# Optimization experiments

Hardware: AMD Instinct MI355X
Metric: run time of the kernel (lower is better)

Reference implementation:

```python
import jax, jax.numpy as jnp
import numpy as np

K = 64  # target active features per sample

def setup_inputs() -> dict:
    key = jax.random.key(0)
    x = jax.random.normal(key, (4096, 24576), dtype=jnp.float32)
    return {"x": x}

def reference(x) -> jnp.ndarray:
    # Training-mode BatchTopK: global threshold = min of top (k * batch) values
    # over the flattened batch, then ReLU(x) gated by (x >= threshold).
    batch_size = x.shape[0]
    total_k = min(K * batch_size, x.size)
    flat = x.reshape(-1)
    topv, _ = jax.lax.top_k(flat, total_k)
    threshold = jax.lax.stop_gradient(topv[-1])  # min of the top-k values (sorted desc)
    return jax.nn.relu(x) * (x >= threshold).astype(x.dtype)
```

## Files before the change

kernel.cpp:

```cpp
#include <hip/hip_runtime.h>

namespace {

struct SelState {
    unsigned forced_fb;
    unsigned bufcount;
    unsigned overflow;
    unsigned sel0;
    unsigned k1;
    unsigned sel1;
    unsigned k2;
};

constexpr int BINS12 = 4096;
constexpr int BINS8  = 256;
constexpr int LCAP   = 2048;
constexpr float GUESS = 2.5f;

using f4v = __attribute__((ext_vector_type(4))) float;

__device__ __forceinline__ unsigned f2key(float f) {
    unsigned u = __float_as_uint(f);
    return (u & 0x80000000u) ? ~u : (u | 0x80000000u);
}
__device__ __forceinline__ float key2f(unsigned k) {
    return __uint_as_float((k & 0x80000000u) ? (k & 0x7fffffffu) : ~k);
}
__device__ __forceinline__ bool is_fb(const SelState* st, unsigned total_k) {
    return st->forced_fb || st->overflow || (st->bufcount < total_k);
}

template <int NB>
__device__ __forceinline__ void scan_desc(const unsigned* __restrict__ hist, unsigned k,
                                          unsigned* __restrict__ lh, unsigned* __restrict__ res) {
    constexpr int CH = NB / 256;
    const int t = threadIdx.x;
    if (t == 0) { res[0] = 0; res[1] = k; }
    unsigned s = 0;
#pragma unroll
    for (int j = 0; j < CH; ++j) {
        unsigned c = hist[NB - 1 - (t * CH + j)];
        lh[t * CH + j] = c;
        s += c;
    }
    __syncthreads();
    const int lane = t & 63, wid = t >> 6;
    unsigned v = s;
#pragma unroll
    for (int d = 1; d < 64; d <<= 1) {
        unsigned u = __shfl_up(v, (unsigned)d, 64);
        if (lane >= d) v += u;
    }
    __shared__ unsigned wp[4];
    if (lane == 63) wp[wid] = v;
    __syncthreads();
    unsigned add = 0;
    for (int w = 0; w < wid; ++w) add += wp[w];
    v += add;
    unsigned pre = v - s;
    if (k > pre && k <= v) {
        unsigned cum = pre;
#pragma unroll
        for (int j = 0; j < CH; ++j) {
            unsigned c = lh[t * CH + j];
            if (cum + c >= k) { res[0] = (unsigned)(NB - 1 - (t * CH + j)); res[1] = k - cum; break; }
            cum += c;
        }
    }
    __syncthreads();
}

__global__ void init_kernel(unsigned* __restrict__ hist0, unsigned* __restrict__ hist1,
                            unsigned* __restrict__ hist2, SelState* __restrict__ st,
                            unsigned force_fb) {
    int t = blockIdx.x * blockDim.x + threadIdx.x;
    int stride = gridDim.x * blockDim.x;
    for (int i = t; i < BINS12; i += stride) { hist0[i] = 0; hist1[i] = 0; }
    if (t < BINS8) hist2[t] = 0;
    if (t == 0) {
        st->forced_fb = force_fb;
        st->bufcount = 0;
        st->overflow = 0;
    }
}

__global__ __launch_bounds__(256) void pass1_kernel(const float* __restrict__ x,
                                                    float* __restrict__ out, long long n,
                                                    unsigned* __restrict__ keys,
                                                    unsigned* __restrict__ idxs,
                                                    unsigned bufcap, SelState* __restrict__ st) {
    if (st->forced_fb) return;
    __shared__ unsigned lkey[LCAP];
    __shared__ unsigned lidx[LCAP];
    __shared__ unsigned lcnt;
    __shared__ unsigned gbase;
    if (threadIdx.x == 0) lcnt = 0;
    __syncthreads();

    const unsigned GKEY = f2key(GUESS);
    long long n4 = n >> 2;
    long long tid = (long long)blockIdx.x * blockDim.x + threadIdx.x;
    long long stride = (long long)gridDim.x * blockDim.x;
    const f4v* xv = (const f4v*)x;
    f4v* ov = (f4v*)out;
    f4v z4 = {0.f, 0.f, 0.f, 0.f};

    for (long long i = tid; i < n4; i += stride) {
        f4v v = __builtin_nontemporal_load(&xv[i]);
        __builtin_nontemporal_store(z4, &ov[i]);
#pragma unroll
        for (int c = 0; c < 4; ++c) {
            unsigned key = f2key(v[c]);
            if (key >= GKEY) {
                unsigned p = atomicAdd(&lcnt, 1u);
                if (p < LCAP) { lkey[p] = key; lidx[p] = (unsigned)((i << 2) + c); }
            }
        }
    }
    for (long long i = (n4 << 2) + tid; i < n; i += stride) {
        float v = x[i];
        out[i] = 0.f;
        unsigned key = f2key(v);
        if (key >= GKEY) {
            unsigned p = atomicAdd(&lcnt, 1u);
            if (p < LCAP) { lkey[p] = key; lidx[p] = (unsigned)i; }
        }
    }

    __syncthreads();
    unsigned cnt = lcnt;
    if (cnt > LCAP) cnt = LCAP;
    if (threadIdx.x == 0) {
        if (lcnt > LCAP) atomicOr(&st->overflow, 1u);
        unsigned base = atomicAdd(&st->bufcount, cnt);
        if (base + cnt > bufcap) atomicOr(&st->overflow, 1u);
        gbase = base;
    }
    __syncthreads();
    unsigned base = gbase;
    for (unsigned i = threadIdx.x; i < cnt; i += 256) {
        unsigned dst = base + i;
        if (dst < bufcap) { keys[dst] = lkey[i]; idxs[dst] = lidx[i]; }
    }
}

__global__ __launch_bounds__(256) void hist0_kernel(const float* __restrict__ x, long long n,
                                                    const unsigned* __restrict__ keys,
                                                    unsigned* __restrict__ hist0,
                                                    const SelState* __restrict__ st,
                                                    unsigned total_k) {
    __shared__ unsigned lh[BINS12];
    for (int i = threadIdx.x; i < BINS12; i += 256) lh[i] = 0;
    __syncthreads();

    long long tid = (long long)blockIdx.x * blockDim.x + threadIdx.x;
    long long stride = (long long)gridDim.x * blockDim.x;

    if (is_fb(st, total_k)) {
        long long n4 = n >> 2;
        const float4* x4 = (const float4*)x;
        for (long long i = tid; i < n4; i += stride) {
            float4 v = x4[i];
            float vv[4] = {v.x, v.y, v.z, v.w};
#pragma unroll
            for (int c = 0; c < 4; ++c) atomicAdd(&lh[f2key(vv[c]) >> 20], 1u);
        }
        for (long long i = (n4 << 2) + tid; i < n; i += stride)
            atomicAdd(&lh[f2key(x[i]) >> 20], 1u);
    } else {
        long long cnt = (long long)st->bufcount;
        long long c4 = cnt >> 2;
        const uint4* k4 = (const uint4*)keys;
        for (long long i = tid; i < c4; i += stride) {
            uint4 kv = k4[i];
            atomicAdd(&lh[kv.x >> 20], 1u);
            atomicAdd(&lh[kv.y >> 20], 1u);
            atomicAdd(&lh[kv.z >> 20], 1u);
            atomicAdd(&lh[kv.w >> 20], 1u);
        }
        for (long long i = (c4 << 2) + tid; i < cnt; i += stride)
            atomicAdd(&lh[keys[i] >> 20], 1u);
    }

    __syncthreads();
    for (int i = threadIdx.x; i < BINS12; i += 256) {
        unsigned c = lh[i];
        if (c) atomicAdd(&hist0[i], c);
    }
}

__global__ __launch_bounds__(256) void hist1_kernel(const float* __restrict__ x, long long n,
                                                    const unsigned* __restrict__ keys,
                                                    const unsigned* __restrict__ hist0,
                                                    unsigned* __restrict__ hist1,
                                                    SelState* __restrict__ st,
                                                    unsigned total_k) {
    __shared__ unsigned lh[BINS12];
    __shared__ unsigned res[2];
    scan_desc<BINS12>(hist0, total_k, lh, res);
    const unsigned sel0 = res[0];
    if (threadIdx.x == 0 && blockIdx.x == 0) { st->sel0 = sel0; st->k1 = res[1]; }

    for (int i = threadIdx.x; i < BINS12; i += 256) lh[i] = 0;
    __syncthreads();

    long long tid = (long long)blockIdx.x * blockDim.x + threadIdx.x;
    long long stride = (long long)gridDim.x * blockDim.x;

    if (is_fb(st, total_k)) {
        long long n4 = n >> 2;
        const float4* x4 = (const float4*)x;
        for (long long i = tid; i < n4; i += stride) {
            float4 v = x4[i];
            float vv[4] = {v.x, v.y, v.z, v.w};
#pragma unroll
            for (int c = 0; c < 4; ++c) {
                unsigned key = f2key(vv[c]);
                if ((key >> 20) == sel0) atomicAdd(&lh[(key >> 8) & 0xFFFu], 1u);
            }
        }
        for (long long i = (n4 << 2) + tid; i < n; i += stride) {
            unsigned key = f2key(x[i]);
            if ((key >> 20) == sel0) atomicAdd(&lh[(key >> 8) & 0xFFFu], 1u);
        }
    } else {
        long long cnt = (long long)st->bufcount;
        long long c4 = cnt >> 2;
        const uint4* k4 = (const uint4*)keys;
        for (long long i = tid; i < c4; i += stride) {
            uint4 kv = k4[i];
            unsigned kk[4] = {kv.x, kv.y, kv.z, kv.w};
#pragma unroll
            for (int c = 0; c < 4; ++c)
                if ((kk[c] >> 20) == sel0) atomicAdd(&lh[(kk[c] >> 8) & 0xFFFu], 1u);
        }
        for (long long i = (c4 << 2) + tid; i < cnt; i += stride) {
            unsigned key = keys[i];
            if ((key >> 20) == sel0) atomicAdd(&lh[(key >> 8) & 0xFFFu], 1u);
        }
    }

    __syncthreads();
    for (int i = threadIdx.x; i < BINS12; i += 256) {
        unsigned c = lh[i];
        if (c) atomicAdd(&hist1[i], c);
    }
}

__global__ __launch_bounds__(256) void hist2_kernel(const float* __restrict__ x, long long n,
                                                    const unsigned* __restrict__ keys,
                                                    const unsigned* __restrict__ hist1,
                                                    unsigned* __restrict__ hist2,
                                                    SelState* __restrict__ st,
                                                    unsigned total_k) {
    __shared__ unsigned lh[BINS12];
    __shared__ unsigned res[2];
    scan_desc<BINS12>(hist1, st->k1, lh, res);
    const unsigned sel1 = (st->sel0 << 12) | res[0];
    if (threadIdx.x == 0 && blockIdx.x == 0) { st->sel1 = sel1; st->k2 = res[1]; }

    for (int i = threadIdx.x; i < BINS8; i += 256) lh[i] = 0;
    __syncthreads();

    long long tid = (long long)blockIdx.x * blockDim.x + threadIdx.x;
    long long stride = (long long)gridDim.x * blockDim.x;

    if (is_fb(st, total_k)) {
        long long n4 = n >> 2;
        const float4* x4 = (const float4*)x;
        for (long long i = tid; i < n4; i += stride) {
            float4 v = x4[i];
            float vv[4] = {v.x, v.y, v.z, v.w};
#pragma unroll
            for (int c = 0; c < 4; ++c) {
                unsigned key = f2key(vv[c]);
                if ((key >> 8) == sel1) atomicAdd(&lh[key & 0xFFu], 1u);
            }
        }
        for (long long i = (n4 << 2) + tid; i < n; i += stride) {
            unsigned key = f2key(x[i]);
            if ((key >> 8) == sel1) atomicAdd(&lh[key & 0xFFu], 1u);
        }
    } else {
        long long cnt = (long long)st->bufcount;
        long long c4 = cnt >> 2;
        const uint4* k4 = (const uint4*)keys;
        for (long long i = tid; i < c4; i += stride) {
            uint4 kv = k4[i];
            unsigned kk[4] = {kv.x, kv.y, kv.z, kv.w};
#pragma unroll
            for (int c = 0; c < 4; ++c)
                if ((kk[c] >> 8) == sel1) atomicAdd(&lh[kk[c] & 0xFFu], 1u);
        }
        for (long long i = (c4 << 2) + tid; i < cnt; i += stride) {
            unsigned key = keys[i];
            if ((key >> 8) == sel1) atomicAdd(&lh[key & 0xFFu], 1u);
        }
    }

    __syncthreads();
    for (int i = threadIdx.x; i < BINS8; i += 256) {
        unsigned c = lh[i];
        if (c) atomicAdd(&hist2[i], c);
    }
}

__global__ __launch_bounds__(256) void gate_kernel(const float* __restrict__ x,
                                                   float* __restrict__ out, long long n,
                                                   const unsigned* __restrict__ keys,
                                                   const unsigned* __restrict__ idxs,
                                                   const unsigned* __restrict__ hist2,
                                                   const SelState* __restrict__ st,
                                                   unsigned total_k) {
    __shared__ unsigned lh[BINS8];
    __shared__ unsigned res[2];
    scan_desc<BINS8>(hist2, st->k2, lh, res);
    const unsigned tkey = (st->sel1 << 8) | res[0];

    long long tid = (long long)blockIdx.x * blockDim.x + threadIdx.x;
    long long stride = (long long)gridDim.x * blockDim.x;

    if (is_fb(st, total_k)) {
        float thr = key2f(tkey);
        long long n4 = n >> 2;
        const float4* x4 = (const float4*)x;
        float4* o4 = (float4*)out;
        for (long long i = tid; i < n4; i += stride) {
            float4 v = x4[i];
            float4 r;
            r.x = (v.x >= thr) ? fmaxf(v.x, 0.f) : 0.f;
            r.y = (v.y >= thr) ? fmaxf(v.y, 0.f) : 0.f;
            r.z = (v.z >= thr) ? fmaxf(v.z, 0.f) : 0.f;
            r.w = (v.w >= thr) ? fmaxf(v.w, 0.f) : 0.f;
            o4[i] = r;
        }
        for (long long i = (n4 << 2) + tid; i < n; i += stride) {
            float v = x[i];
            out[i] = (v >= thr) ? fmaxf(v, 0.f) : 0.f;
        }
    } else {
        long long cnt = (long long)st->bufcount;
        for (long long i = tid; i < cnt; i += stride) {
            unsigned kk = keys[i];
            if (kk >= tkey) out[idxs[i]] = key2f(kk);
        }
    }
}

}

extern "C" void kernel_launch(void* const* d_in, const int* in_sizes, int n_in,
                              void* d_out, int out_size, void* d_ws, size_t ws_size,
                              hipStream_t stream) {
    const float* x = (const float*)d_in[0];
    float* out = (float*)d_out;
    long long n = (long long)in_sizes[0];

    long long tk = 64LL * 4096LL;
    if (tk > n) tk = n;
    unsigned total_k = (unsigned)tk;

    char* ws = (char*)d_ws;
    unsigned* hist0 = (unsigned*)(ws);
    unsigned* hist1 = (unsigned*)(ws + 16384);
    unsigned* hist2 = (unsigned*)(ws + 32768);
    SelState* st    = (SelState*)(ws + 33792);

    unsigned bufcap = 0;
    unsigned* keys = (unsigned*)(ws + 65536);
    unsigned* idxs = nullptr;
    if (ws_size > 65536) {
        size_t avail = (ws_size - 65536) / 8;
        size_t cap = avail > 16u * 1024u * 1024u ? 16u * 1024u * 1024u : avail;
        bufcap = (unsigned)(cap & ~3ull);
        idxs = keys + bufcap;
    }
    unsigned force_fb = (bufcap < 2u * total_k || n > 0xFFFF0000LL) ? 1u : 0u;

    const int blocks = 2048;

    init_kernel<<<16, 256, 0, stream>>>(hist0, hist1, hist2, st, force_fb);
    pass1_kernel<<<blocks, 256, 0, stream>>>(x, out, n, keys, idxs, bufcap, st);
    hist0_kernel<<<blocks, 256, 0, stream>>>(x, n, keys, hist0, st, total_k);
    hist1_kernel<<<blocks, 256, 0, stream>>>(x, n, keys, hist0, hist1, st, total_k);
    hist2_kernel<<<blocks, 256, 0, stream>>>(x, n, keys, hist1, hist2, st, total_k);
    gate_kernel<<<blocks, 256, 0, stream>>>(x, out, n, keys, idxs, hist2, st, total_k);
}
```

Baseline: 209.7 us.

## Fuse top-bin histogram into candidate pass and zero output via memset

The first-level 12-bit histogram is now built inside the candidate-collection pass using a shared-memory histogram, so the separate pass over the candidate buffer is no longer needed on the fast path. The fallback path keeps its own histogram kernel, which writes to a separate buffer, and hist1 chooses which of the two to scan. Output zeroing moves out of pass1 into a hipMemsetAsync, so pass1 now only reads the input. The trade-off is an extra 16 KB of LDS per block in pass1, which may lower occupancy, and an extra fill operation on the stream.

```diff
diff --git a/kernel.cpp b/kernel.cpp
--- a/kernel.cpp
+++ b/kernel.cpp
@@ -70,12 +70,12 @@
     __syncthreads();
 }
 
-__global__ void init_kernel(unsigned* __restrict__ hist0, unsigned* __restrict__ hist1,
-                            unsigned* __restrict__ hist2, SelState* __restrict__ st,
-                            unsigned force_fb) {
+__global__ void init_kernel(unsigned* __restrict__ hist0s, unsigned* __restrict__ hist0f,
+                            unsigned* __restrict__ hist1, unsigned* __restrict__ hist2,
+                            SelState* __restrict__ st, unsigned force_fb) {
     int t = blockIdx.x * blockDim.x + threadIdx.x;
     int stride = gridDim.x * blockDim.x;
-    for (int i = t; i < BINS12; i += stride) { hist0[i] = 0; hist1[i] = 0; }
+    for (int i = t; i < BINS12; i += stride) { hist0s[i] = 0; hist0f[i] = 0; hist1[i] = 0; }
     if (t < BINS8) hist2[t] = 0;
     if (t == 0) {
         st->forced_fb = force_fb;
@@ -84,16 +84,19 @@
     }
 }
 
-__global__ __launch_bounds__(256) void pass1_kernel(const float* __restrict__ x,
-                                                    float* __restrict__ out, long long n,
+__global__ __launch_bounds__(256) void pass1_kernel(const float* __restrict__ x, long long n,
                                                     unsigned* __restrict__ keys,
                                                     unsigned* __restrict__ idxs,
-                                                    unsigned bufcap, SelState* __restrict__ st) {
+                                                    unsigned bufcap,
+                                                    unsigned* __restrict__ hist0s,
+                                                    SelState* __restrict__ st) {
     if (st->forced_fb) return;
     __shared__ unsigned lkey[LCAP];
     __shared__ unsigned lidx[LCAP];
+    __shared__ unsigned lhist[BINS12];
     __shared__ unsigned lcnt;
     __shared__ unsigned gbase;
+    for (int i = threadIdx.x; i < BINS12; i += 256) lhist[i] = 0;
     if (threadIdx.x == 0) lcnt = 0;
     __syncthreads();
 
@@ -102,28 +105,25 @@
     long long tid = (long long)blockIdx.x * blockDim.x + threadIdx.x;
     long long stride = (long long)gridDim.x * blockDim.x;
     const f4v* xv = (const f4v*)x;
-    f4v* ov = (f4v*)out;
-    f4v z4 = {0.f, 0.f, 0.f, 0.f};
 
     for (long long i = tid; i < n4; i += stride) {
         f4v v = __builtin_nontemporal_load(&xv[i]);
-        __builtin_nontemporal_store(z4, &ov[i]);
 #pragma unroll
         for (int c = 0; c < 4; ++c) {
             unsigned key = f2key(v[c]);
             if (key >= GKEY) {
                 unsigned p = atomicAdd(&lcnt, 1u);
                 if (p < LCAP) { lkey[p] = key; lidx[p] = (unsigned)((i << 2) + c); }
+                atomicAdd(&lhist[key >> 20], 1u);
             }
         }
     }
     for (long long i = (n4 << 2) + tid; i < n; i += stride) {
-        float v = x[i];
-        out[i] = 0.f;
-        unsigned key = f2key(v);
+        unsigned key = f2key(x[i]);
         if (key >= GKEY) {
             unsigned p = atomicAdd(&lcnt, 1u);
             if (p < LCAP) { lkey[p] = key; lidx[p] = (unsigned)i; }
+            atomicAdd(&lhist[key >> 20], 1u);
         }
     }
 
@@ -142,62 +142,50 @@
         unsigned dst = base + i;
         if (dst < bufcap) { keys[dst] = lkey[i]; idxs[dst] = lidx[i]; }
     }
-}
-
-__global__ __launch_bounds__(256) void hist0_kernel(const float* __restrict__ x, long long n,
-                                                    const unsigned* __restrict__ keys,
-                                                    unsigned* __restrict__ hist0,
-                                                    const SelState* __restrict__ st,
-                                                    unsigned total_k) {
+    for (int i = threadIdx.x; i < BINS12; i += 256) {
+        unsigned c = lhist[i];
+        if (c) atomicAdd(&hist0s[i], c);
+    }
+}
+
+__global__ __launch_bounds__(256) void fb_hist0_kernel(const float* __restrict__ x, long long n,
+                                                       unsigned* __restrict__ hist0f,
+                                                       const SelState* __restrict__ st,
+                                                       unsigned total_k) {
+    if (!is_fb(st, total_k)) return;
     __shared__ unsigned lh[BINS12];
     for (int i = threadIdx.x; i < BINS12; i += 256) lh[i] = 0;
     __syncthreads();
-
-    long long tid = (long long)blockIdx.x * blockDim.x + threadIdx.x;
-    long long stride = (long long)gridDim.x * blockDim.x;
-
-    if (is_fb(st, total_k)) {
-        long long n4 = n >> 2;
-        const float4* x4 = (const float4*)x;
-        for (long long i = tid; i < n4; i += stride) {
-            float4 v = x4[i];
-            float vv[4] = {v.x, v.y, v.z, v.w};
-#pragma unroll
-            for (int c = 0; c < 4; ++c) atomicAdd(&lh[f2key(vv[c]) >> 20], 1u);
-        }
-        for (long long i = (n4 << 2) + tid; i < n; i += stride)
-            atomicAdd(&lh[f2key(x[i]) >> 20], 1u);
-    } else {
-        long long cnt = (long long)st->bufcount;
-        long long c4 = cnt >> 2;
-        const uint4* k4 = (const uint4*)keys;
-        for (long long i = tid; i < c4; i += stride) {
-            uint4 kv = k4[i];
-            atomicAdd(&lh[kv.x >> 20], 1u);
-            atomicAdd(&lh[kv.y >> 20], 1u);
-            atomicAdd(&lh[kv.z >> 20], 1u);
-            atomicAdd(&lh[kv.w >> 20], 1u);
-        }
-        for (long long i = (c4 << 2) + tid; i < cnt; i += stride)
-            atomicAdd(&lh[keys[i] >> 20], 1u);
-    }
-
+    long long n4 = n >> 2;
+    long long tid = (long long)blockIdx.x * blockDim.x + threadIdx.x;
+    long long stride = (long long)gridDim.x * blockDim.x;
+    const float4* x4 = (const float4*)x;
+    for (long long i = tid; i < n4; i += stride) {
+        float4 v = x4[i];
+        float vv[4] = {v.x, v.y, v.z, v.w};
+#pragma unroll
+        for (int c = 0; c < 4; ++c) atomicAdd(&lh[f2key(vv[c]) >> 20], 1u);
+    }
+    for (long long i = (n4 << 2) + tid; i < n; i += stride)
+        atomicAdd(&lh[f2key(x[i]) >> 20], 1u);
     __syncthreads();
     for (int i = threadIdx.x; i < BINS12; i += 256) {
         unsigned c = lh[i];
-        if (c) atomicAdd(&hist0[i], c);
+        if (c) atomicAdd(&hist0f[i], c);
     }
 }
 
 __global__ __launch_bounds__(256) void hist1_kernel(const float* __restrict__ x, long long n,
                                                     const unsigned* __restrict__ keys,
-                                                    const unsigned* __restrict__ hist0,
+                                                    const unsigned* __restrict__ hist0s,
+                                                    const unsigned* __restrict__ hist0f,
                                                     unsigned* __restrict__ hist1,
                                                     SelState* __restrict__ st,
                                                     unsigned total_k) {
     __shared__ unsigned lh[BINS12];
     __shared__ unsigned res[2];
-    scan_desc<BINS12>(hist0, total_k, lh, res);
+    const bool fb = is_fb(st, total_k);
+    scan_desc<BINS12>(fb ? hist0f : hist0s, total_k, lh, res);
     const unsigned sel0 = res[0];
     if (threadIdx.x == 0 && blockIdx.x == 0) { st->sel0 = sel0; st->k1 = res[1]; }
 
@@ -207,7 +195,7 @@
     long long tid = (long long)blockIdx.x * blockDim.x + threadIdx.x;
     long long stride = (long long)gridDim.x * blockDim.x;
 
-    if (is_fb(st, total_k)) {
+    if (fb) {
         long long n4 = n >> 2;
         const float4* x4 = (const float4*)x;
         for (long long i = tid; i < n4; i += stride) {
@@ -361,10 +349,11 @@
     unsigned total_k = (unsigned)tk;
 
     char* ws = (char*)d_ws;
-    unsigned* hist0 = (unsigned*)(ws);
-    unsigned* hist1 = (unsigned*)(ws + 16384);
-    unsigned* hist2 = (unsigned*)(ws + 32768);
-    SelState* st    = (SelState*)(ws + 33792);
+    unsigned* hist0s = (unsigned*)(ws);
+    unsigned* hist0f = (unsigned*)(ws + 16384);
+    unsigned* hist1  = (unsigned*)(ws + 32768);
+    unsigned* hist2  = (unsigned*)(ws + 49152);
+    SelState* st     = (SelState*)(ws + 50176);
 
     unsigned bufcap = 0;
     unsigned* keys = (unsigned*)(ws + 65536);
@@ -379,10 +368,11 @@
 
     const int blocks = 2048;
 
-    init_kernel<<<16, 256, 0, stream>>>(hist0, hist1, hist2, st, force_fb);
-    pass1_kernel<<<blocks, 256, 0, stream>>>(x, out, n, keys, idxs, bufcap, st);
-    hist0_kernel<<<blocks, 256, 0, stream>>>(x, n, keys, hist0, st, total_k);
-    hist1_kernel<<<blocks, 256, 0, stream>>>(x, n, keys, hist0, hist1, st, total_k);
+    hipMemsetAsync(out, 0, (size_t)n * sizeof(float), stream);
+    init_kernel<<<16, 256, 0, stream>>>(hist0s, hist0f, hist1, hist2, st, force_fb);
+    pass1_kernel<<<blocks, 256, 0, stream>>>(x, n, keys, idxs, bufcap, hist0s, st);
+    fb_hist0_kernel<<<blocks, 256, 0, stream>>>(x, n, hist0f, st, total_k);
+    hist1_kernel<<<blocks, 256, 0, stream>>>(x, n, keys, hist0s, hist0f, hist1, st, total_k);
     hist2_kernel<<<blocks, 256, 0, stream>>>(x, n, keys, hist1, hist2, st, total_k);
     gate_kernel<<<blocks, 256, 0, stream>>>(x, out, n, keys, idxs, hist2, st, total_k);
 }
```

After: 211.5 us. No clear change (+0.9%).

## Fuse radix-select pipeline into one cooperative kernel with grid syncs

Applied to the files above, without the earlier changes.

Replaces the six-kernel chain (init, candidate gather, three histogram passes, gate) with a single cooperative persistent kernel that uses grid.sync between phases. Each block redoes the histogram prefix scans locally instead of passing selections through global state. The output zeroing is split from the candidate scan into its own store loop. Launch overhead and inter-kernel gaps go away, at the cost of grid-wide barriers and a grid limited to the resident block count. The old chain is kept as a fallback if the cooperative launch fails.

```diff
diff --git a/kernel.cpp b/kernel.cpp
--- a/kernel.cpp
+++ b/kernel.cpp
@@ -1,4 +1,7 @@
 #include <hip/hip_runtime.h>
+#include <hip/hip_cooperative_groups.h>
+
+namespace cg = cooperative_groups;
 
 namespace {
 
@@ -70,6 +73,208 @@
     __syncthreads();
 }
 
+template <int SHIFT, int MASK>
+__device__ __forceinline__ void hist_accum_x(const float* __restrict__ x, long long n,
+                                             unsigned sel, int selshift,
+                                             unsigned* __restrict__ lh,
+                                             long long tid, long long stride) {
+    long long n4 = n >> 2;
+    const float4* x4 = (const float4*)x;
+    for (long long i = tid; i < n4; i += stride) {
+        float4 v = x4[i];
+        float vv[4] = {v.x, v.y, v.z, v.w};
+#pragma unroll
+        for (int c = 0; c < 4; ++c) {
+            unsigned key = f2key(vv[c]);
+            if (selshift == 32 || (key >> selshift) == sel)
+                atomicAdd(&lh[(key >> SHIFT) & MASK], 1u);
+        }
+    }
+    for (long long i = (n4 << 2) + tid; i < n; i += stride) {
+        unsigned key = f2key(x[i]);
+        if (selshift == 32 || (key >> selshift) == sel)
+            atomicAdd(&lh[(key >> SHIFT) & MASK], 1u);
+    }
+}
+template <int SHIFT, int MASK>
+__device__ __forceinline__ void hist_accum_keys(const unsigned* __restrict__ keys, long long cnt,
+                                                unsigned sel, int selshift,
+                                                unsigned* __restrict__ lh,
+                                                long long tid, long long stride) {
+    long long c4 = cnt >> 2;
+    const uint4* k4 = (const uint4*)keys;
+    for (long long i = tid; i < c4; i += stride) {
+        uint4 kv = k4[i];
+        unsigned kk[4] = {kv.x, kv.y, kv.z, kv.w};
+#pragma unroll
+        for (int c = 0; c < 4; ++c)
+            if (selshift == 32 || (kk[c] >> selshift) == sel)
+                atomicAdd(&lh[(kk[c] >> SHIFT) & MASK], 1u);
+    }
+    for (long long i = (c4 << 2) + tid; i < cnt; i += stride) {
+        unsigned key = keys[i];
+        if (selshift == 32 || (key >> selshift) == sel)
+            atomicAdd(&lh[(key >> SHIFT) & MASK], 1u);
+    }
+}
+
+__global__ __launch_bounds__(256, 4) void mega_kernel(
+    const float* __restrict__ x, float* __restrict__ out, long long n,
+    unsigned* __restrict__ keys, unsigned* __restrict__ idxs, unsigned bufcap,
+    unsigned* __restrict__ hist0, unsigned* __restrict__ hist1,
+    unsigned* __restrict__ hist2, SelState* __restrict__ st,
+    unsigned total_k, unsigned force_fb) {
+    cg::grid_group grid = cg::this_grid();
+    __shared__ unsigned smem[BINS12];
+    unsigned* lkey = smem;
+    unsigned* lidx = smem + LCAP;
+    unsigned* lh   = smem;
+    __shared__ unsigned lcnt, gbase, sfb, scnt;
+    __shared__ unsigned res[2];
+
+    const int t = threadIdx.x;
+    const long long tid = (long long)blockIdx.x * blockDim.x + t;
+    const long long stride = (long long)gridDim.x * blockDim.x;
+
+    for (long long i = tid; i < BINS12; i += stride) { hist0[i] = 0; hist1[i] = 0; }
+    for (long long i = tid; i < BINS8; i += stride) hist2[i] = 0;
+    if (tid == 0) { st->bufcount = 0; st->overflow = 0; }
+    grid.sync();
+
+    {
+        f4v z = {0.f, 0.f, 0.f, 0.f};
+        long long n4 = n >> 2;
+        f4v* ov = (f4v*)out;
+        for (long long i = tid; i < n4; i += stride) __builtin_nontemporal_store(z, &ov[i]);
+        for (long long i = (n4 << 2) + tid; i < n; i += stride) out[i] = 0.f;
+    }
+    if (!force_fb) {
+        if (t == 0) lcnt = 0;
+        __syncthreads();
+        const unsigned GKEY = f2key(GUESS);
+        long long n8 = n >> 3;
+        const f4v* xv = (const f4v*)x;
+        for (long long i = tid; i < n8; i += stride) {
+            f4v a = __builtin_nontemporal_load(&xv[2 * i]);
+            f4v b = __builtin_nontemporal_load(&xv[2 * i + 1]);
+#pragma unroll
+            for (int c = 0; c < 4; ++c) {
+                unsigned key = f2key(a[c]);
+                if (key >= GKEY) {
+                    unsigned p = atomicAdd(&lcnt, 1u);
+                    if (p < LCAP) { lkey[p] = key; lidx[p] = (unsigned)((i << 3) + c); }
+                }
+            }
+#pragma unroll
+            for (int c = 0; c < 4; ++c) {
+                unsigned key = f2key(b[c]);
+                if (key >= GKEY) {
+                    unsigned p = atomicAdd(&lcnt, 1u);
+                    if (p < LCAP) { lkey[p] = key; lidx[p] = (unsigned)((i << 3) + 4 + c); }
+                }
+            }
+        }
+        for (long long i = (n8 << 3) + tid; i < n; i += stride) {
+            unsigned key = f2key(x[i]);
+            if (key >= GKEY) {
+                unsigned p = atomicAdd(&lcnt, 1u);
+                if (p < LCAP) { lkey[p] = key; lidx[p] = (unsigned)i; }
+            }
+        }
+        __syncthreads();
+        unsigned cnt = lcnt > LCAP ? LCAP : lcnt;
+        if (t == 0) {
+            if (lcnt > LCAP) atomicOr(&st->overflow, 1u);
+            unsigned base = atomicAdd(&st->bufcount, cnt);
+            if (base + cnt > bufcap) atomicOr(&st->overflow, 1u);
+            gbase = base;
+        }
+        __syncthreads();
+        unsigned base = gbase;
+        for (unsigned i = t; i < cnt; i += 256) {
+            unsigned dst = base + i;
+            if (dst < bufcap) { keys[dst] = lkey[i]; idxs[dst] = lidx[i]; }
+        }
+    }
+    grid.sync();
+
+    if (t == 0) {
+        unsigned ov = atomicOr(&st->overflow, 0u);
+        unsigned bc = atomicAdd(&st->bufcount, 0u);
+        sfb = (force_fb || ov || bc < total_k) ? 1u : 0u;
+        scnt = bc < bufcap ? bc : bufcap;
+    }
+    __syncthreads();
+    const bool fb = (sfb != 0u);
+    const long long cnt = (long long)scnt;
+
+    for (int i = t; i < BINS12; i += 256) lh[i] = 0;
+    __syncthreads();
+    if (fb) hist_accum_x<20, 0xFFF>(x, n, 0, 32, lh, tid, stride);
+    else    hist_accum_keys<20, 0xFFF>(keys, cnt, 0, 32, lh, tid, stride);
+    __syncthreads();
+    for (int i = t; i < BINS12; i += 256) {
+        unsigned c = lh[i];
+        if (c) atomicAdd(&hist0[i], c);
+    }
+    grid.sync();
+
+    scan_desc<BINS12>(hist0, total_k, lh, res);
+    const unsigned sel0 = res[0];
+    const unsigned k1 = res[1];
+    for (int i = t; i < BINS12; i += 256) lh[i] = 0;
+    __syncthreads();
+    if (fb) hist_accum_x<8, 0xFFF>(x, n, sel0, 20, lh, tid, stride);
+    else    hist_accum_keys<8, 0xFFF>(keys, cnt, sel0, 20, lh, tid, stride);
+    __syncthreads();
+    for (int i = t; i < BINS12; i += 256) {
+        unsigned c = lh[i];
+        if (c) atomicAdd(&hist1[i], c);
+    }
+    grid.sync();
+
+    scan_desc<BINS12>(hist1, k1, lh, res);
+    const unsigned sel1 = (sel0 << 12) | res[0];
+    const unsigned k2 = res[1];
+    for (int i = t; i < BINS8; i += 256) lh[i] = 0;
+    __syncthreads();
+    if (fb) hist_accum_x<0, 0xFF>(x, n, sel1, 8, lh, tid, stride);
+    else    hist_accum_keys<0, 0xFF>(keys, cnt, sel1, 8, lh, tid, stride);
+    __syncthreads();
+    for (int i = t; i < BINS8; i += 256) {
+        unsigned c = lh[i];
+        if (c) atomicAdd(&hist2[i], c);
+    }
+    grid.sync();
+
+    scan_desc<BINS8>(hist2, k2, lh, res);
+    const unsigned tkey = (sel1 << 8) | res[0];
+    if (fb) {
+        float thr = key2f(tkey);
+        long long n4 = n >> 2;
+        const float4* x4 = (const float4*)x;
+        float4* o4 = (float4*)out;
+        for (long long i = tid; i < n4; i += stride) {
+            float4 v = x4[i];
+            float4 r;
+            r.x = (v.x >= thr) ? fmaxf(v.x, 0.f) : 0.f;
+            r.y = (v.y >= thr) ? fmaxf(v.y, 0.f) : 0.f;
+            r.z = (v.z >= thr) ? fmaxf(v.z, 0.f) : 0.f;
+            r.w = (v.w >= thr) ? fmaxf(v.w, 0.f) : 0.f;
+            o4[i] = r;
+        }
+        for (long long i = (n4 << 2) + tid; i < n; i += stride) {
+            float v = x[i];
+            out[i] = (v >= thr) ? fmaxf(v, 0.f) : 0.f;
+        }
+    } else {
+        for (long long i = tid; i < cnt; i += stride) {
+            unsigned kk = keys[i];
+            if (kk >= tkey) out[idxs[i]] = key2f(kk);
+        }
+    }
+}
+
 __global__ void init_kernel(unsigned* __restrict__ hist0, unsigned* __restrict__ hist1,
                             unsigned* __restrict__ hist2, SelState* __restrict__ st,
                             unsigned force_fb) {
@@ -77,26 +282,19 @@
     int stride = gridDim.x * blockDim.x;
     for (int i = t; i < BINS12; i += stride) { hist0[i] = 0; hist1[i] = 0; }
     if (t < BINS8) hist2[t] = 0;
-    if (t == 0) {
-        st->forced_fb = force_fb;
-        st->bufcount = 0;
-        st->overflow = 0;
-    }
-}
-
-__global__ __launch_bounds__(256) void pass1_kernel(const float* __restrict__ x,
-                                                    float* __restrict__ out, long long n,
-                                                    unsigned* __restrict__ keys,
-                                                    unsigned* __restrict__ idxs,
-                                                    unsigned bufcap, SelState* __restrict__ st) {
-    if (st->forced_fb) return;
+    if (t == 0) { st->forced_fb = force_fb; st->bufcount = 0; st->overflow = 0; }
+}
+
+__global__ __launch_bounds__(256) void pass1_chain(const float* __restrict__ x,
+                                                   float* __restrict__ out, long long n,
+                                                   unsigned* __restrict__ keys,
+                                                   unsigned* __restrict__ idxs,
+                                                   unsigned bufcap, SelState* __restrict__ st) {
     __shared__ unsigned lkey[LCAP];
     __shared__ unsigned lidx[LCAP];
-    __shared__ unsigned lcnt;
-    __shared__ unsigned gbase;
+    __shared__ unsigned lcnt, gbase;
     if (threadIdx.x == 0) lcnt = 0;
     __syncthreads();
-
     const unsigned GKEY = f2key(GUESS);
     long long n4 = n >> 2;
     long long tid = (long long)blockIdx.x * blockDim.x + threadIdx.x;
@@ -104,7 +302,6 @@
     const f4v* xv = (const f4v*)x;
     f4v* ov = (f4v*)out;
     f4v z4 = {0.f, 0.f, 0.f, 0.f};
-
     for (long long i = tid; i < n4; i += stride) {
         f4v v = __builtin_nontemporal_load(&xv[i]);
         __builtin_nontemporal_store(z4, &ov[i]);
@@ -126,10 +323,8 @@
             if (p < LCAP) { lkey[p] = key; lidx[p] = (unsigned)i; }
         }
     }
-
-    __syncthreads();
-    unsigned cnt = lcnt;
-    if (cnt > LCAP) cnt = LCAP;
+    __syncthreads();
+    unsigned cnt = lcnt > LCAP ? LCAP : lcnt;
     if (threadIdx.x == 0) {
         if (lcnt > LCAP) atomicOr(&st->overflow, 1u);
         unsigned base = atomicAdd(&st->bufcount, cnt);
@@ -144,44 +339,18 @@
     }
 }
 
-__global__ __launch_bounds__(256) void hist0_kernel(const float* __restrict__ x, long long n,
-                                                    const unsigned* __restrict__ keys,
-                                                    unsigned* __restrict__ hist0,
-                                                    const SelState* __restrict__ st,
-                                                    unsigned total_k) {
+__global__ __launch_bounds__(256) void hist0_chain(const float* __restrict__ x, long long n,
+                                                   const unsigned* __restrict__ keys,
+                                                   unsigned* __restrict__ hist0,
+                                                   const SelState* __restrict__ st,
+                                                   unsigned total_k) {
     __shared__ unsigned lh[BINS12];
     for (int i = threadIdx.x; i < BINS12; i += 256) lh[i] = 0;
     __syncthreads();
-
     long long tid = (long long)blockIdx.x * blockDim.x + threadIdx.x;
     long long stride = (long long)gridDim.x * blockDim.x;
-
-    if (is_fb(st, total_k)) {
-        long long n4 = n >> 2;
-        const float4* x4 = (const float4*)x;
-        for (long long i = tid; i < n4; i += stride) {
-            float4 v = x4[i];
-            float vv[4] = {v.x, v.y, v.z, v.w};
-#pragma unroll
-            for (int c = 0; c < 4; ++c) atomicAdd(&lh[f2key(vv[c]) >> 20], 1u);
-        }
-        for (long long i = (n4 << 2) + tid; i < n; i += stride)
-            atomicAdd(&lh[f2key(x[i]) >> 20], 1u);
-    } else {
-        long long cnt = (long long)st->bufcount;
-        long long c4 = cnt >> 2;
-        const uint4* k4 = (const uint4*)keys;
-        for (long long i = tid; i < c4; i += stride) {
-            uint4 kv = k4[i];
-            atomicAdd(&lh[kv.x >> 20], 1u);
-            atomicAdd(&lh[kv.y >> 20], 1u);
-            atomicAdd(&lh[kv.z >> 20], 1u);
-            atomicAdd(&lh[kv.w >> 20], 1u);
-        }
-        for (long long i = (c4 << 2) + tid; i < cnt; i += stride)
-            atomicAdd(&lh[keys[i] >> 20], 1u);
-    }
-
+    if (is_fb(st, total_k)) hist_accum_x<20, 0xFFF>(x, n, 0, 32, lh, tid, stride);
+    else hist_accum_keys<20, 0xFFF>(keys, (long long)(st->bufcount < 0x7FFFFFFFu ? st->bufcount : 0), 0, 32, lh, tid, stride);
     __syncthreads();
     for (int i = threadIdx.x; i < BINS12; i += 256) {
         unsigned c = lh[i];
@@ -189,57 +358,23 @@
     }
 }
 
-__global__ __launch_bounds__(256) void hist1_kernel(const float* __restrict__ x, long long n,
-                                                    const unsigned* __restrict__ keys,
-                                                    const unsigned* __restrict__ hist0,
-                                                    unsigned* __restrict__ hist1,
-                                                    SelState* __restrict__ st,
-                                                    unsigned total_k) {
+__global__ __launch_bounds__(256) void hist1_chain(const float* __restrict__ x, long long n,
+                                                   const unsigned* __restrict__ keys,
+                                                   const unsigned* __restrict__ hist0,
+                                                   unsigned* __restrict__ hist1,
+                                                   SelState* __restrict__ st,
+                                                   unsigned total_k) {
     __shared__ unsigned lh[BINS12];
     __shared__ unsigned res[2];
     scan_desc<BINS12>(hist0, total_k, lh, res);
     const unsigned sel0 = res[0];
     if (threadIdx.x == 0 && blockIdx.x == 0) { st->sel0 = sel0; st->k1 = res[1]; }
-
     for (int i = threadIdx.x; i < BINS12; i += 256) lh[i] = 0;
     __syncthreads();
-
     long long tid = (long long)blockIdx.x * blockDim.x + threadIdx.x;
     long long stride = (long long)gridDim.x * blockDim.x;
-
-    if (is_fb(st, total_k)) {
-        long long n4 = n >> 2;
-        const float4* x4 = (const float4*)x;
-        for (long long i = tid; i < n4; i += stride) {
-            float4 v = x4[i];
-            float vv[4] = {v.x, v.y, v.z, v.w};
-#pragma unroll
-            for (int c = 0; c < 4; ++c) {
-                unsigned key = f2key(vv[c]);
-                if ((key >> 20) == sel0) atomicAdd(&lh[(key >> 8) & 0xFFFu], 1u);
-            }
-        }
-        for (long long i = (n4 << 2) + tid; i < n; i += stride) {
-            unsigned key = f2key(x[i]);
-            if ((key >> 20) == sel0) atomicAdd(&lh[(key >> 8) & 0xFFFu], 1u);
-        }
-    } else {
-        long long cnt = (long long)st->bufcount;
-        long long c4 = cnt >> 2;
-        const uint4* k4 = (const uint4*)keys;
-        for (long long i = tid; i < c4; i += stride) {
-            uint4 kv = k4[i];
-            unsigned kk[4] = {kv.x, kv.y, kv.z, kv.w};
-#pragma unroll
-            for (int c = 0; c < 4; ++c)
-                if ((kk[c] >> 20) == sel0) atomicAdd(&lh[(kk[c] >> 8) & 0xFFFu], 1u);
-        }
-        for (long long i = (c4 << 2) + tid; i < cnt; i += stride) {
-            unsigned key = keys[i];
-            if ((key >> 20) == sel0) atomicAdd(&lh[(key >> 8) & 0xFFFu], 1u);
-        }
-    }
-
+    if (is_fb(st, total_k)) hist_accum_x<8, 0xFFF>(x, n, sel0, 20, lh, tid, stride);
+    else hist_accum_keys<8, 0xFFF>(keys, (long long)st->bufcount, sel0, 20, lh, tid, stride);
     __syncthreads();
     for (int i = threadIdx.x; i < BINS12; i += 256) {
         unsigned c = lh[i];
@@ -247,57 +382,23 @@
     }
 }
 
-__global__ __launch_bounds__(256) void hist2_kernel(const float* __restrict__ x, long long n,
-                                                    const unsigned* __restrict__ keys,
-                                                    const unsigned* __restrict__ hist1,
-                                                    unsigned* __restrict__ hist2,
-                                                    SelState* __restrict__ st,
-                                                    unsigned total_k) {
+__global__ __launch_bounds__(256) void hist2_chain(const float* __restrict__ x, long long n,
+                                                   const unsigned* __restrict__ keys,
+                                                   const unsigned* __restrict__ hist1,
+                                                   unsigned* __restrict__ hist2,
+                                                   SelState* __restrict__ st,
+                                                   unsigned total_k) {
     __shared__ unsigned lh[BINS12];
     __shared__ unsigned res[2];
     scan_desc<BINS12>(hist1, st->k1, lh, res);
     const unsigned sel1 = (st->sel0 << 12) | res[0];
     if (threadIdx.x == 0 && blockIdx.x == 0) { st->sel1 = sel1; st->k2 = res[1]; }
-
     for (int i = threadIdx.x; i < BINS8; i += 256) lh[i] = 0;
     __syncthreads();
-
     long long tid = (long long)blockIdx.x * blockDim.x + threadIdx.x;
     long long stride = (long long)gridDim.x * blockDim.x;
-
-    if (is_fb(st, total_k)) {
-        long long n4 = n >> 2;
-        const float4* x4 = (const float4*)x;
-        for (long long i = tid; i < n4; i += stride) {
-            float4 v = x4[i];
-            float vv[4] = {v.x, v.y, v.z, v.w};
-#pragma unroll
-            for (int c = 0; c < 4; ++c) {
-                unsigned key = f2key(vv[c]);
-                if ((key >> 8) == sel1) atomicAdd(&lh[key & 0xFFu], 1u);
-            }
-        }
-        for (long long i = (n4 << 2) + tid; i < n; i += stride) {
-            unsigned key = f2key(x[i]);
-            if ((key >> 8) == sel1) atomicAdd(&lh[key & 0xFFu], 1u);
-        }
-    } else {
-        long long cnt = (long long)st->bufcount;
-        long long c4 = cnt >> 2;
-        const uint4* k4 = (const uint4*)keys;
-        for (long long i = tid; i < c4; i += stride) {
-            uint4 kv = k4[i];
-            unsigned kk[4] = {kv.x, kv.y, kv.z, kv.w};
-#pragma unroll
-            for (int c = 0; c < 4; ++c)
-                if ((kk[c] >> 8) == sel1) atomicAdd(&lh[kk[c] & 0xFFu], 1u);
-        }
-        for (long long i = (c4 << 2) + tid; i < cnt; i += stride) {
-            unsigned key = keys[i];
-            if ((key >> 8) == sel1) atomicAdd(&lh[key & 0xFFu], 1u);
-        }
-    }
-
+    if (is_fb(st, total_k)) hist_accum_x<0, 0xFF>(x, n, sel1, 8, lh, tid, stride);
+    else hist_accum_keys<0, 0xFF>(keys, (long long)st->bufcount, sel1, 8, lh, tid, stride);
     __syncthreads();
     for (int i = threadIdx.x; i < BINS8; i += 256) {
         unsigned c = lh[i];
@@ -305,21 +406,19 @@
     }
 }
 
-__global__ __launch_bounds__(256) void gate_kernel(const float* __restrict__ x,
-                                                   float* __restrict__ out, long long n,
-                                                   const unsigned* __restrict__ keys,
-                                                   const unsigned* __restrict__ idxs,
-                                                   const unsigned* __restrict__ hist2,
-                                                   const SelState* __restrict__ st,
-                                                   unsigned total_k) {
+__global__ __launch_bounds__(256) void gate_chain(const float* __restrict__ x,
+                                                  float* __restrict__ out, long long n,
+                                                  const unsigned* __restrict__ keys,
+                                                  const unsigned* __restrict__ idxs,
+                                                  const unsigned* __restrict__ hist2,
+                                                  const SelState* __restrict__ st,
+                                                  unsigned total_k) {
     __shared__ unsigned lh[BINS8];
     __shared__ unsigned res[2];
     scan_desc<BINS8>(hist2, st->k2, lh, res);
     const unsigned tkey = (st->sel1 << 8) | res[0];
-
     long long tid = (long long)blockIdx.x * blockDim.x + threadIdx.x;
     long long stride = (long long)gridDim.x * blockDim.x;
-
     if (is_fb(st, total_k)) {
         float thr = key2f(tkey);
         long long n4 = n >> 2;
@@ -377,12 +476,29 @@
     }
     unsigned force_fb = (bufcap < 2u * total_k || n > 0xFFFF0000LL) ? 1u : 0u;
 
+    int dev = 0;
+    hipGetDevice(&dev);
+    int cus = 0;
+    hipDeviceGetAttribute(&cus, hipDeviceAttributeMultiprocessorCount, dev);
+    int maxb = 0;
+    hipOccupancyMaxActiveBlocksPerMultiprocessor(&maxb, (const void*)mega_kernel, 256, 0);
+    long long capacity = (long long)maxb * (long long)cus;
+
+    if (capacity >= 256) {
+        int grid = (int)(capacity > 4096 ? 4096 : capacity);
+        void* args[] = {(void*)&x, (void*)&out, (void*)&n, (void*)&keys, (void*)&idxs,
+                        (void*)&bufcap, (void*)&hist0, (void*)&hist1, (void*)&hist2,
+                        (void*)&st, (void*)&total_k, (void*)&force_fb};
+        hipError_t e = hipLaunchCooperativeKernel((const void*)mega_kernel, dim3(grid),
+                                                  dim3(256), args, 0, stream);
+        if (e == hipSuccess) return;
+    }
+
     const int blocks = 2048;
-
     init_kernel<<<16, 256, 0, stream>>>(hist0, hist1, hist2, st, force_fb);
-    pass1_kernel<<<blocks, 256, 0, stream>>>(x, out, n, keys, idxs, bufcap, st);
-    hist0_kernel<<<blocks, 256, 0, stream>>>(x, n, keys, hist0, st, total_k);
-    hist1_kernel<<<blocks, 256, 0, stream>>>(x, n, keys, hist0, hist1, st, total_k);
-    hist2_kernel<<<blocks, 256, 0, stream>>>(x, n, keys, hist1, hist2, st, total_k);
-    gate_kernel<<<blocks, 256, 0, stream>>>(x, out, n, keys, idxs, hist2, st, total_k);
-}
+    pass1_chain<<<blocks, 256, 0, stream>>>(x, out, n, keys, idxs, bufcap, st);
+    hist0_chain<<<blocks, 256, 0, stream>>>(x, n, keys, hist0, st, total_k);
+    hist1_chain<<<blocks, 256, 0, stream>>>(x, n, keys, hist0, hist1, st, total_k);
+    hist2_chain<<<blocks, 256, 0, stream>>>(x, n, keys, hist1, hist2, st, total_k);
+    gate_chain<<<blocks, 256, 0, stream>>>(x, out, n, keys, idxs, hist2, st, total_k);
+}
```

Result: slower. 572.7 us (+173.1%).
